# Kernel tuning notes

Measured on AMD Instinct MI355X. Metric: run time of the kernel, lower is better.

## Reference

```python
import jax, jax.numpy as jnp
import numpy as np

L = 4096   # num_tokens (one prefill sequence)
D = 2048   # hidden_size
HK = 16    # num_k_heads
HV = 32    # num_v_heads
DK = 128   # head_k_dim
DV = 128   # head_v_dim
RATIO = HV // HK
EPS = 1e-6


def setup_inputs() -> dict:
    key = jax.random.key(0)
    ks = jax.random.split(key, 11)
    s = 0.02
    return {
        "hidden_states": jax.random.normal(ks[0], (L, D), jnp.float32),
        "Wq": jax.random.normal(ks[1], (D, HK * DK), jnp.float32) * s,
        "Wk": jax.random.normal(ks[2], (D, HK * DK), jnp.float32) * s,
        "Wv": jax.random.normal(ks[3], (D, HV * DV), jnp.float32) * s,
        "Wz": jax.random.normal(ks[4], (D, HV * DV), jnp.float32) * s,
        "Wb": jax.random.normal(ks[5], (D, HV), jnp.float32) * s,
        "Wa": jax.random.normal(ks[6], (D, HV), jnp.float32) * s,
        "A_log": jnp.log(jax.random.uniform(ks[7], (HV,), jnp.float32, 1.0, 16.0)),
        "dt_bias": jax.random.normal(ks[8], (HV,), jnp.float32) * 0.5,
        "norm_weight": jnp.ones((DV,), jnp.float32),
        "W_out": jax.random.normal(ks[9], (HV * DV, D), jnp.float32) * s,
    }


def _l2norm(x):
    return x * jax.lax.rsqrt(jnp.sum(x * x, axis=-1, keepdims=True) + EPS)


def reference(hidden_states, Wq, Wk, Wv, Wz, Wb, Wa, A_log, dt_bias, norm_weight, W_out):
    h = hidden_states
    # --- input projections (qkvz + ba split) ---
    q = _l2norm((h @ Wq).reshape(L, HK, DK))            # [L, HK, DK]
    k = _l2norm((h @ Wk).reshape(L, HK, DK))
    v = (h @ Wv).reshape(L, HV, DV)                     # [L, HV, DV]
    z = (h @ Wz).reshape(L, HV, DV)                     # gate for RMSNorm
    beta = jax.nn.sigmoid(h @ Wb)                       # [L, HV]
    g = -jnp.exp(A_log) * jax.nn.softplus(h @ Wa + dt_bias)  # [L, HV]
    decay = jnp.exp(g)                                  # per-token per-head decay
    # repeat shared q/k heads to value heads (GQA ratio)
    q = jnp.repeat(q, RATIO, axis=1) * (DK ** -0.5)     # [L, HV, DK]
    k = jnp.repeat(k, RATIO, axis=1)

    # --- gated delta rule recurrence over tokens ---
    def step(S, xs):
        q_t, k_t, v_t, b_t, d_t = xs                    # [HV,DK],[HV,DK],[HV,DV],[HV],[HV]
        S = S * d_t[:, None, None]                      # decay state [HV, DK, DV]
        pred = jnp.einsum('hk,hkv->hv', k_t, S)         # memory readout
        delta = (v_t - pred) * b_t[:, None]             # delta-rule correction
        S = S + k_t[:, :, None] * delta[:, None, :]
        o = jnp.einsum('hk,hkv->hv', q_t, S)
        return S, o

    S0 = jnp.zeros((HV, DK, DV), jnp.float32)
    _, core = jax.lax.scan(step, S0, (q, k, v, beta, decay))  # core: [L, HV, DV]

    # --- gated RMSNorm: x * silu(z), rms-normalize over head dim ---
    x = core * jax.nn.silu(z)
    x = x * jax.lax.rsqrt(jnp.mean(x * x, axis=-1, keepdims=True) + EPS) * norm_weight

    # --- output projection ---
    return x.reshape(L, HV * DV) @ W_out                # [L, D]
```

## Files before the change

### kernel.cpp

```cpp
#include <hip/hip_runtime.h>

#define LTOK 4096
#define DHID 2048
#define HKN  16
#define HVN  32
#define DKK  128
#define NTOT 12288

typedef unsigned short u16;
typedef __attribute__((ext_vector_type(8))) short short8;
typedef __attribute__((ext_vector_type(8))) unsigned short u16x8;
typedef __attribute__((ext_vector_type(4))) unsigned short u16x4;
typedef __attribute__((ext_vector_type(4))) float f32x4;

__device__ __forceinline__ float b2f(u16 u) {
  unsigned int x = ((unsigned int)u) << 16;
  return __builtin_bit_cast(float, x);
}
__device__ __forceinline__ u16 f2bf(float f) {
  unsigned int u = __builtin_bit_cast(unsigned int, f);
  u += 0x7FFFu + ((u >> 16) & 1u);
  return (u16)(u >> 16);
}

template<int C> __device__ __forceinline__ float dppmv(float x) {
  int i = __builtin_amdgcn_update_dpp(0, __builtin_bit_cast(int, x), C, 0xF, 0xF, true);
  return __builtin_bit_cast(float, i);
}
__device__ __forceinline__ float red16(float x) {
  x += dppmv<0xB1>(x);
  x += dppmv<0x4E>(x);
  x += dppmv<0x124>(x);
  x += dppmv<0x128>(x);
  return x;
}

__device__ __forceinline__ void gld16(const void* g, void* l) {
  __builtin_amdgcn_global_load_lds((const __attribute__((address_space(1))) void*)g,
                                   (__attribute__((address_space(3))) void*)l, 16, 0, 0);
}

__device__ __forceinline__ int sw16(int r, int c, int rowc) { return (r * rowc + c) ^ ((r & 7) << 3); }

__device__ __forceinline__ void cstore(u16* C, size_t i, float v) { C[i] = f2bf(v); }
__device__ __forceinline__ void cstore(float* C, size_t i, float v) { C[i] = v; }

__global__ __launch_bounds__(256)
void k_cvt(const float* __restrict__ s, u16* __restrict__ d, int n) {
  const int i = (blockIdx.x * 256 + threadIdx.x) * 4;
  const float4 v = *(const float4*)(s + i);
  ushort4 o;
  o.x = f2bf(v.x); o.y = f2bf(v.y); o.z = f2bf(v.z); o.w = f2bf(v.w);
  *(ushort4*)(d + i) = o;
}

__global__ __launch_bounds__(256)
void k_tr(const float* __restrict__ src, u16* __restrict__ dst, int R, int C) {
  __shared__ float tl[32][33];
  const int r0 = blockIdx.y * 32, c0 = blockIdx.x * 32;
  const int tr = threadIdx.x >> 3, tc = (threadIdx.x & 7) * 4;
  const float4 v = *(const float4*)(src + (size_t)(r0 + tr) * C + c0 + tc);
  tl[tr][tc] = v.x; tl[tr][tc + 1] = v.y; tl[tr][tc + 2] = v.z; tl[tr][tc + 3] = v.w;
  __syncthreads();
  ushort4 o;
  o.x = f2bf(tl[tc + 0][tr]); o.y = f2bf(tl[tc + 1][tr]);
  o.z = f2bf(tl[tc + 2][tr]); o.w = f2bf(tl[tc + 3][tr]);
  *(ushort4*)(dst + (size_t)(c0 + tr) * R + r0 + tc) = o;
}

template<typename OutT>
__global__ __launch_bounds__(256, 2)
void k_gemm(const u16* __restrict__ A, const u16* __restrict__ Bt, OutT* __restrict__ C,
            int M, int N, int K) {
  __shared__ u16 lA[128 * 32];
  __shared__ u16 lB[128 * 32];
  const int tid = threadIdx.x;
  const int lane = tid & 63, wid = tid >> 6;
  const int nt = blockIdx.x, mt = blockIdx.y;
  const int wm = (wid >> 1) * 64, wn = (wid & 1) * 64;
  const size_t sK = (size_t)K;
  const u16* aS = A + (size_t)(mt * 128 + wid * 32 + (lane >> 2)) * sK + (lane & 3) * 8;
  const u16* bS = Bt + (size_t)(nt * 128 + wid * 32 + (lane >> 2)) * sK + (lane & 3) * 8;
  u16* lAw = lA + wid * 1024;
  u16* lBw = lB + wid * 1024;
  f32x4 acc[4][4] = {};
  const int aoff = (lane & 15) * 32 + (lane >> 4) * 8;

  for (int k0 = 0; k0 < K; k0 += 32) {
    gld16(aS + k0, lAw);
    gld16(aS + k0 + 16 * sK, lAw + 512);
    gld16(bS + k0, lBw);
    gld16(bS + k0 + 16 * sK, lBw + 512);
    __syncthreads();
    short8 af[4], bfv[4];
#pragma unroll
    for (int i = 0; i < 4; ++i) {
      af[i]  = *(const short8*)&lA[(wm + i * 16) * 32 + aoff];
      bfv[i] = *(const short8*)&lB[(wn + i * 16) * 32 + aoff];
    }
#pragma unroll
    for (int i = 0; i < 4; ++i)
#pragma unroll
      for (int j = 0; j < 4; ++j)
        acc[i][j] = __builtin_amdgcn_mfma_f32_16x16x32_bf16(af[i], bfv[j], acc[i][j], 0, 0, 0);
    __syncthreads();
  }
  const int r0 = mt * 128 + wm + (lane >> 4) * 4;
  const int c0 = nt * 128 + wn + (lane & 15);
#pragma unroll
  for (int i = 0; i < 4; ++i)
#pragma unroll
    for (int j = 0; j < 4; ++j)
#pragma unroll
      for (int e = 0; e < 4; ++e)
        cstore(C, (size_t)(r0 + i * 16 + e) * N + c0 + j * 16, acc[i][j][e]);
}

__global__ __launch_bounds__(256)
void k_ba(const float* __restrict__ h, const float* __restrict__ Wb, const float* __restrict__ Wa,
          const float* __restrict__ A_log, const float* __restrict__ dtb,
          float* __restrict__ beta, float* __restrict__ g_out) {
  const int w = threadIdx.x >> 6, lane = threadIdx.x & 63;
  const int t = blockIdx.x * 4 + w;
  const int j = lane & 31;
  const bool isB = lane < 32;
  const float* __restrict__ hr = h + (size_t)t * DHID;
  const float* Wc = isB ? Wb : Wa;
  float acc = 0.f;
  for (int kk = 0; kk < DHID; ++kk) acc = fmaf(hr[kk], Wc[(size_t)kk * HVN + j], acc);
  if (isB) {
    beta[(size_t)t * HVN + j] = 1.f / (1.f + expf(-acc));
  } else {
    float xx = acc + dtb[j];
    float sp = (xx > 20.f) ? xx : log1pf(expf(xx));
    g_out[(size_t)t * HVN + j] = -expf(A_log[j]) * sp;
  }
}

__global__ __launch_bounds__(256)
void k_l2n(u16* __restrict__ qkvz) {
  const int w = threadIdx.x >> 6, lane = threadIdx.x & 63;
  const int r = blockIdx.x * 4 + w;
  const int isK = r >> 16;
  const int rr = r & 65535;
  const int t = rr >> 4, hd = rr & 15;
  u16* p = qkvz + (size_t)t * NTOT + isK * 2048 + hd * DKK + lane * 2;
  float a = b2f(p[0]), b = b2f(p[1]);
  float ss = a * a + b * b;
  ss = red16(ss);
  ss += __shfl_xor(ss, 16);
  ss += __shfl_xor(ss, 32);
  const float sc = rsqrtf(ss + 1e-6f) * (isK ? 1.f : 0.08838834764831845f);
  p[0] = f2bf(a * sc); p[1] = f2bf(b * sc);
}

#define MFMA16(a, b, c) __builtin_amdgcn_mfma_f32_16x16x32_bf16(a, b, c, 0, 0, 0)

__global__ __launch_bounds__(256)
void k_r1(const u16* __restrict__ qkvz, const float* __restrict__ beta_g,
          const float* __restrict__ g_g, u16* __restrict__ UM_g, float* __restrict__ cumL_g) {
  const int pair = blockIdx.x;
  const int hv = pair >> 6, n = pair & 63;
  const int hk = hv >> 1;
  const int t0 = n * 64;
  const int tid = threadIdx.x, lane = tid & 63, wv = tid >> 6;
  const int fr = lane & 15, fq = lane >> 4;

  __shared__ __align__(16) u16 Xb[256 * 64];
  __shared__ __align__(16) u16 Dbuf0[64 * 64 * 2];
  __shared__ __align__(16) u16 Dbuf1[64 * 64 * 2];
  __shared__ float Lc[64];
  __shared__ float Bc[64];
  u16* Kl = Dbuf0;

  const int j = tid & 63, h = tid >> 6;
  const u16* kg = qkvz + (size_t)(t0 + j) * NTOT + 2048 + hk * DKK + h * 32;
  const u16* vg = qkvz + (size_t)(t0 + j) * NTOT + 4096 + hv * DKK + h * 32;
  u16x8 kv[4], vv[4];
#pragma unroll
  for (int i = 0; i < 4; ++i) { kv[i] = *(const u16x8*)(kg + i * 8); vv[i] = *(const u16x8*)(vg + i * 8); }
  if (tid < 64) {
    Lc[tid] = g_g[(size_t)(t0 + tid) * HVN + hv];
    Bc[tid] = beta_g[(size_t)(t0 + tid) * HVN + hv];
  }
#pragma unroll
  for (int i = 0; i < 4; ++i) *(u16x8*)&Kl[sw16(j, h * 32 + i * 8, 128)] = kv[i];
  __syncthreads();
  if (tid == 0) { float a = 0.f; for (int t = 0; t < 64; ++t) { a += Lc[t]; Lc[t] = a; } }
  __syncthreads();
  if (tid < 64) cumL_g[(size_t)pair * 64 + tid] = Lc[tid];

  {
    const float bj = Bc[j];
    const float mj = bj * __expf(Lc[j]);
#pragma unroll
    for (int i = 0; i < 4; ++i)
#pragma unroll
      for (int e = 0; e < 8; ++e) {
        int c = h * 32 + i * 8 + e;
        Xb[sw16(c, j, 64)] = f2bf(bj * b2f(vv[i][e]));
        Xb[sw16(128 + c, j, 64)] = f2bf(mj * b2f(kv[i][e]));
      }
  }
  f32x4 kk[4] = {};
#pragma unroll
  for (int ks = 0; ks < 4; ++ks) {
    short8 afr = *(const short8*)&Kl[sw16(wv * 16 + fr, ks * 32 + fq * 8, 128)];
#pragma unroll
    for (int ct = 0; ct < 4; ++ct) {
      short8 bfr = *(const short8*)&Kl[sw16(ct * 16 + fr, ks * 32 + fq * 8, 128)];
      kk[ct] = MFMA16(afr, bfr, kk[ct]);
    }
  }
  __syncthreads();

  f32x4 acc[16];
#pragma unroll
  for (int ct = 0; ct < 16; ++ct) {
    u16x4 xi = *(const u16x4*)&Xb[sw16(ct * 16 + fr, wv * 16 + fq * 4, 64)];
    acc[ct][0] = b2f(xi[0]); acc[ct][1] = b2f(xi[1]); acc[ct][2] = b2f(xi[2]); acc[ct][3] = b2f(xi[3]);
  }
#pragma unroll
  for (int ct = 0; ct < 4; ++ct) {
    const int s = ct * 16 + fr;
    u16x4 pk;
#pragma unroll
    for (int e = 0; e < 4; ++e) {
      const int t = wv * 16 + fq * 4 + e;
      float v = (s < t) ? -Bc[t] * __expf(Lc[t] - Lc[s]) * kk[ct][e] : 0.f;
      pk[e] = f2bf(v);
      Dbuf0[sw16(t, s, 64)] = pk[e];
    }
    *(u16x4*)&Dbuf0[4096 + sw16(s, wv * 16 + fq * 4, 64)] = pk;
  }
  __syncthreads();

  u16* DA = Dbuf0;
  u16* DB = Dbuf1;
  for (int stg = 0; stg < 6; ++stg) {
    u16* Dr = DA;
    u16* Dc = DA + 4096;
    short8 da0 = *(const short8*)&Dr[sw16(wv * 16 + fr, 0 + fq * 8, 64)];
    short8 da1 = *(const short8*)&Dr[sw16(wv * 16 + fr, 32 + fq * 8, 64)];
#pragma unroll
    for (int ct = 0; ct < 16; ++ct) {
      short8 b0 = *(const short8*)&Xb[sw16(ct * 16 + fr, 0 + fq * 8, 64)];
      short8 b1 = *(const short8*)&Xb[sw16(ct * 16 + fr, 32 + fq * 8, 64)];
      acc[ct] = MFMA16(da0, b0, acc[ct]);
      acc[ct] = MFMA16(da1, b1, acc[ct]);
    }
    f32x4 sq[4] = {};
    if (stg < 5) {
#pragma unroll
      for (int ct = 0; ct < 4; ++ct) {
        short8 sb0 = *(const short8*)&Dc[sw16(ct * 16 + fr, 0 + fq * 8, 64)];
        short8 sb1 = *(const short8*)&Dc[sw16(ct * 16 + fr, 32 + fq * 8, 64)];
        sq[ct] = MFMA16(da0, sb0, sq[ct]);
        sq[ct] = MFMA16(da1, sb1, sq[ct]);
      }
    }
    __syncthreads();
#pragma unroll
    for (int ct = 0; ct < 16; ++ct) {
      u16x4 pk;
      pk[0] = f2bf(acc[ct][0]); pk[1] = f2bf(acc[ct][1]); pk[2] = f2bf(acc[ct][2]); pk[3] = f2bf(acc[ct][3]);
      *(u16x4*)&Xb[sw16(ct * 16 + fr, wv * 16 + fq * 4, 64)] = pk;
    }
    if (stg < 5) {
#pragma unroll
      for (int ct = 0; ct < 4; ++ct) {
        u16x4 pk;
        pk[0] = f2bf(sq[ct][0]); pk[1] = f2bf(sq[ct][1]); pk[2] = f2bf(sq[ct][2]); pk[3] = f2bf(sq[ct][3]);
        *(u16x4*)&(DB + 4096)[sw16(ct * 16 + fr, wv * 16 + fq * 4, 64)] = pk;
#pragma unroll
        for (int e = 0; e < 4; ++e) DB[sw16(wv * 16 + fq * 4 + e, ct * 16 + fr, 64)] = pk[e];
      }
    }
    __syncthreads();
    u16* tmp = DA; DA = DB; DB = tmp;
  }

#pragma unroll
  for (int ct = 0; ct < 16; ++ct) {
    const int c = ct * 16 + fr;
#pragma unroll
    for (int e = 0; e < 4; ++e) {
      const int t = wv * 16 + fq * 4 + e;
      float v = acc[ct][e];
      if (ct >= 8) v = -v;
      UM_g[((size_t)pair * 64 + t) * 256 + c] = f2bf(v);
    }
  }
}

__global__ __launch_bounds__(512)
void k_r2(u16* __restrict__ qkvz, const u16* __restrict__ UM_g,
          const float* __restrict__ cumL_g, u16* __restrict__ o1_g) {
  const int hv = blockIdx.x >> 1, cs = blockIdx.x & 1;
  const int hk = hv >> 1;
  const int tid = threadIdx.x, lane = tid & 63, w = tid >> 6;
  const int fr = lane & 15, fq = lane >> 4;
  const int j = tid & 63, h = tid >> 6;

  __shared__ __align__(16) u16 Ml2[2][8192];
  __shared__ __align__(16) u16 Ql2[2][8192];
  __shared__ __align__(16) u16 Kt2[2][8192];
  __shared__ __align__(16) u16 Ul2[2][4096];
  __shared__ __align__(16) u16 dT[4096];
  __shared__ __align__(16) u16 SbT[8192];
  __shared__ __align__(16) u16 o1b[4096];
  __shared__ float Lc2[2][64];

  const int tw = w & 3;
  const int d0 = (w >> 2) * 2;

  f32x4 sacc[4];
#pragma unroll
  for (int d = 0; d < 4; ++d) sacc[d] = (f32x4){0.f, 0.f, 0.f, 0.f};
  for (int i = tid; i < 8192; i += 512) SbT[i] = 0;

  u16x8 pQ0, pQ1, pK0, pK1, pM0, pM1, pU0;
  float pL, pL63;

#define PREF(nn) {                                                            \
    const int nc = ((nn) < 64) ? (nn) : 63;                                   \
    const int pr = hv * 64 + nc; const int tt0 = nc * 64;                     \
    const u16* qg = qkvz + (size_t)(tt0 + j) * NTOT + hk * DKK + h * 16;      \
    pQ0 = *(const u16x8*)qg;          pQ1 = *(const u16x8*)(qg + 8);          \
    pK0 = *(const u16x8*)(qg + 2048); pK1 = *(const u16x8*)(qg + 2056);       \
    const u16* mg = UM_g + ((size_t)pr * 64 + j) * 256;                       \
    pM0 = *(const u16x8*)(mg + 128 + h * 16);                                 \
    pM1 = *(const u16x8*)(mg + 136 + h * 16);                                 \
    pU0 = *(const u16x8*)(mg + cs * 64 + h * 8);                              \
    pL = cumL_g[(size_t)pr * 64 + j]; pL63 = cumL_g[(size_t)pr * 64 + 63]; }

#define STW(b) {                                                              \
    *(u16x8*)&Ql2[b][sw16(j, h * 16, 128)] = pQ0;                             \
    *(u16x8*)&Ql2[b][sw16(j, h * 16 + 8, 128)] = pQ1;                         \
    *(u16x8*)&Ml2[b][sw16(j, h * 16, 128)] = pM0;                             \
    *(u16x8*)&Ml2[b][sw16(j, h * 16 + 8, 128)] = pM1;                         \
    const float scK = __expf(pL63 - pL);                                      \
    _Pragma("unroll")                                                         \
    for (int e = 0; e < 8; ++e) {                                             \
      Kt2[b][sw16(h * 16 + e, j, 64)] = f2bf(scK * b2f(pK0[e]));              \
      Kt2[b][sw16(h * 16 + 8 + e, j, 64)] = f2bf(scK * b2f(pK1[e]));          \
      Ul2[b][sw16(h * 8 + e, j, 64)] = pU0[e];                                \
    }                                                                         \
    if (h == 0) Lc2[b][j] = pL; }

  PREF(0)
  STW(0)
  __syncthreads();

  for (int n = 0; n < 64; ++n) {
    const int cur = n & 1;
    const int pair = hv * 64 + n, t0 = n * 64;
    const float curL63 = pL63;
    PREF(n + 1)

    short8 amf[4], aqf[4];
#pragma unroll
    for (int ks = 0; ks < 4; ++ks) {
      amf[ks] = *(const short8*)&Ml2[cur][sw16(tw * 16 + fr, ks * 32 + fq * 8, 128)];
      aqf[ks] = *(const short8*)&Ql2[cur][sw16(tw * 16 + fr, ks * 32 + fq * 8, 128)];
    }
    float el[4];
#pragma unroll
    for (int e = 0; e < 4; ++e) el[e] = __expf(Lc2[cur][tw * 16 + fq * 4 + e]);
#pragma unroll
    for (int dd = 0; dd < 2; ++dd) {
      const int d = d0 + dd;
      u16x4 uv = *(const u16x4*)&Ul2[cur][sw16(d * 16 + fr, tw * 16 + fq * 4, 64)];
      f32x4 dc;
      dc[0] = b2f(uv[0]); dc[1] = b2f(uv[1]); dc[2] = b2f(uv[2]); dc[3] = b2f(uv[3]);
      f32x4 oc = {};
#pragma unroll
      for (int ks = 0; ks < 4; ++ks) {
        short8 bs = *(const short8*)&SbT[sw16(d * 16 + fr, ks * 32 + fq * 8, 128)];
        dc = MFMA16(amf[ks], bs, dc);
        oc = MFMA16(aqf[ks], bs, oc);
      }
      u16x4 pk;
      pk[0] = f2bf(dc[0]); pk[1] = f2bf(dc[1]); pk[2] = f2bf(dc[2]); pk[3] = f2bf(dc[3]);
      *(u16x4*)&dT[sw16(d * 16 + fr, tw * 16 + fq * 4, 64)] = pk;
#pragma unroll
      for (int e = 0; e < 4; ++e)
        o1b[sw16(tw * 16 + fq * 4 + e, d * 16 + fr, 64)] = f2bf(oc[e] * el[e]);
    }
    __syncthreads();

    {
      const int i = tid * 8;
      u16x8 vd = *(const u16x8*)&dT[i];
      const int f = cs * 4096 + i;
      *(u16x8*)(qkvz + (size_t)(t0 + (f >> 7)) * NTOT + 4096 + hv * DKK + (f & 127)) = vd;
      u16x8 vo = *(const u16x8*)&o1b[i];
      *(u16x8*)(o1_g + (size_t)pair * 8192 + (size_t)(i >> 6) * 128 + cs * 64 + (i & 63)) = vo;
    }
    STW(cur ^ 1)
    {
      const float eC = __expf(curL63);
      short8 ak0 = *(const short8*)&Kt2[cur][sw16(w * 16 + fr, fq * 8, 64)];
      short8 ak1 = *(const short8*)&Kt2[cur][sw16(w * 16 + fr, 32 + fq * 8, 64)];
#pragma unroll
      for (int d = 0; d < 4; ++d) {
        short8 bd0 = *(const short8*)&dT[sw16(d * 16 + fr, fq * 8, 64)];
        short8 bd1 = *(const short8*)&dT[sw16(d * 16 + fr, 32 + fq * 8, 64)];
        f32x4 sa = sacc[d];
#pragma unroll
        for (int e = 0; e < 4; ++e) sa[e] *= eC;
        sa = MFMA16(ak0, bd0, sa);
        sa = MFMA16(ak1, bd1, sa);
        sacc[d] = sa;
        u16x4 pk;
        pk[0] = f2bf(sa[0]); pk[1] = f2bf(sa[1]); pk[2] = f2bf(sa[2]); pk[3] = f2bf(sa[3]);
        *(u16x4*)&SbT[sw16(d * 16 + fr, w * 16 + fq * 4, 128)] = pk;
      }
    }
    __syncthreads();
  }
#undef PREF
#undef STW
}

__global__ __launch_bounds__(512)
void k_r3(const u16* __restrict__ qkvz, const u16* __restrict__ o1_g,
          const float* __restrict__ cumL_g, const float* __restrict__ nw,
          u16* __restrict__ x) {
  const int pair = blockIdx.x, hv = pair >> 6, n = pair & 63, hk = hv >> 1, t0 = n * 64;
  const int tid = threadIdx.x, lane = tid & 63, w = tid >> 6;
  const int fr = lane & 15, fq = lane >> 4;
  const int j = tid & 63, h = tid >> 6;

  __shared__ __align__(16) u16 Ql[8192];
  __shared__ __align__(16) u16 Kl[8192];
  __shared__ __align__(16) u16 Gl[4096];
  __shared__ __align__(16) u16 dTl[8192];
  __shared__ __align__(16) float of[64 * 132];
  __shared__ float Lc[64];
  __shared__ float Lw[128];

  {
    const u16* qg = qkvz + (size_t)(t0 + j) * NTOT + hk * DKK + h * 16;
    u16x8 q0 = *(const u16x8*)qg, q1 = *(const u16x8*)(qg + 8);
    u16x8 k0 = *(const u16x8*)(qg + 2048), k1 = *(const u16x8*)(qg + 2056);
    *(u16x8*)&Ql[sw16(j, h * 16, 128)] = q0;
    *(u16x8*)&Ql[sw16(j, h * 16 + 8, 128)] = q1;
    *(u16x8*)&Kl[sw16(j, h * 16, 128)] = k0;
    *(u16x8*)&Kl[sw16(j, h * 16 + 8, 128)] = k1;
  }
#pragma unroll
  for (int it = 0; it < 2; ++it) {
    const int f = ((w * 2 + it) * 64 + lane) * 8;
    gld16(qkvz + (size_t)(t0 + (f >> 7)) * NTOT + 4096 + hv * DKK + (f & 127),
          (char*)dTl + (w * 2 + it) * 1024);
  }
  if (tid < 64) Lc[tid] = cumL_g[(size_t)pair * 64 + tid];
  if (tid < 128) Lw[tid] = nw[tid];
  __syncthreads();

  const int tw = w & 3, sp = (w >> 2) * 2;
  {
    f32x4 kk0 = {}, kk1 = {};
#pragma unroll
    for (int ks = 0; ks < 4; ++ks) {
      short8 aq = *(const short8*)&Ql[sw16(tw * 16 + fr, ks * 32 + fq * 8, 128)];
      short8 b0 = *(const short8*)&Kl[sw16(sp * 16 + fr, ks * 32 + fq * 8, 128)];
      short8 b1 = *(const short8*)&Kl[sw16((sp + 1) * 16 + fr, ks * 32 + fq * 8, 128)];
      kk0 = MFMA16(aq, b0, kk0);
      kk1 = MFMA16(aq, b1, kk1);
    }
#pragma unroll
    for (int e = 0; e < 4; ++e) {
      const int t = tw * 16 + fq * 4 + e;
      const float Lt = Lc[t];
      const int s0 = sp * 16 + fr, s1 = s0 + 16;
      Gl[sw16(t, s0, 64)] = f2bf((s0 <= t) ? kk0[e] * __expf(Lt - Lc[s0]) : 0.f);
      Gl[sw16(t, s1, 64)] = f2bf((s1 <= t) ? kk1[e] * __expf(Lt - Lc[s1]) : 0.f);
    }
  }
  __syncthreads();

  {
    short8 ag0 = *(const short8*)&Gl[sw16(tw * 16 + fr, fq * 8, 64)];
    short8 ag1 = *(const short8*)&Gl[sw16(tw * 16 + fr, 32 + fq * 8, 64)];
#pragma unroll
    for (int dd = 0; dd < 4; ++dd) {
      const int d = (w >> 2) * 4 + dd;
      short8 bd0 = *(const short8*)&dTl[sw16(d * 16 + fr, fq * 8, 64)];
      short8 bd1 = *(const short8*)&dTl[sw16(d * 16 + fr, 32 + fq * 8, 64)];
      f32x4 oc = {};
      oc = MFMA16(ag0, bd0, oc);
      oc = MFMA16(ag1, bd1, oc);
#pragma unroll
      for (int e = 0; e < 4; ++e) of[(tw * 16 + fq * 4 + e) * 132 + d * 16 + fr] = oc[e];
    }
  }
  __syncthreads();

  {
    const int t = tid >> 3, q8 = tid & 7;
    const u16* zp = qkvz + (size_t)(t0 + t) * NTOT + 8192 + hv * DKK + q8 * 16;
    const u16* op = o1_g + (size_t)pair * 8192 + t * 128;
    float xv[16];
    float ss = 0.f;
#pragma unroll
    for (int i = 0; i < 2; ++i) {
      u16x8 zv = *(const u16x8*)(zp + i * 8);
      u16x8 ov = *(const u16x8*)(op + (((q8 * 16 + i * 8) ^ ((t & 7) << 3))));
#pragma unroll
      for (int e = 0; e < 8; ++e) {
        float z = b2f(zv[e]);
        float o = of[t * 132 + q8 * 16 + i * 8 + e] + b2f(ov[e]);
        float xx = o * (z / (1.f + __expf(-z)));
        xv[i * 8 + e] = xx;
        ss = fmaf(xx, xx, ss);
      }
    }
    ss += __shfl_xor(ss, 1);
    ss += __shfl_xor(ss, 2);
    ss += __shfl_xor(ss, 4);
    const float scl = rsqrtf(ss * (1.f / 128.f) + 1e-6f);
    u16* xo = x + (size_t)(t0 + t) * 4096 + hv * DKK + q8 * 16;
#pragma unroll
    for (int i = 0; i < 2; ++i) {
      u16x8 pk;
#pragma unroll
      for (int e = 0; e < 8; ++e) pk[e] = f2bf(xv[i * 8 + e] * scl * Lw[q8 * 16 + i * 8 + e]);
      *(u16x8*)(xo + i * 8) = pk;
    }
  }
}

extern "C" void kernel_launch(void* const* d_in, const int* in_sizes, int n_in,
                              void* d_out, int out_size, void* d_ws, size_t ws_size,
                              hipStream_t stream) {
  const float* h    = (const float*)d_in[0];
  const float* Wq   = (const float*)d_in[1];
  const float* Wk   = (const float*)d_in[2];
  const float* Wv   = (const float*)d_in[3];
  const float* Wz   = (const float*)d_in[4];
  const float* Wb   = (const float*)d_in[5];
  const float* Wa   = (const float*)d_in[6];
  const float* Alog = (const float*)d_in[7];
  const float* dtb  = (const float*)d_in[8];
  const float* nw   = (const float*)d_in[9];
  const float* Wo   = (const float*)d_in[10];
  char* ws = (char*)d_ws;
  u16* h_bf  = (u16*)(ws);
  u16* Wt    = (u16*)(ws + 16777216ull);
  u16* UM    = (u16*)(ws);
  u16* Wto   = (u16*)(ws + 67108864ull);
  u16* qkvz  = (u16*)(ws + 83886080ull);
  u16* o1g   = (u16*)(ws + 184549376ull);
  u16* xbuf  = (u16*)(ws + 16777216ull);
  float* beta  = (float*)(ws + 218103808ull);
  float* g     = (float*)(ws + 218103808ull + 524288ull);
  float* cumL  = (float*)(ws + 218103808ull + 1048576ull);

  k_cvt<<<8192, 256, 0, stream>>>(h, h_bf, LTOK * DHID);
  k_tr<<<dim3(64, 64), 256, 0, stream>>>(Wq, Wt, 2048, 2048);
  k_tr<<<dim3(64, 64), 256, 0, stream>>>(Wk, Wt + 2048ull * 2048, 2048, 2048);
  k_tr<<<dim3(128, 64), 256, 0, stream>>>(Wv, Wt + 4096ull * 2048, 2048, 4096);
  k_tr<<<dim3(128, 64), 256, 0, stream>>>(Wz, Wt + 8192ull * 2048, 2048, 4096);
  k_tr<<<dim3(64, 128), 256, 0, stream>>>(Wo, Wto, 4096, 2048);
  k_gemm<u16><<<dim3(96, 32), 256, 0, stream>>>(h_bf, Wt, qkvz, 4096, 12288, 2048);
  k_ba<<<1024, 256, 0, stream>>>(h, Wb, Wa, Alog, dtb, beta, g);
  k_l2n<<<32768, 256, 0, stream>>>(qkvz);
  k_r1<<<2048, 256, 0, stream>>>(qkvz, beta, g, UM, cumL);
  k_r2<<<64, 512, 0, stream>>>(qkvz, UM, cumL, o1g);
  k_r3<<<2048, 512, 0, stream>>>(qkvz, o1g, cumL, nw, xbuf);
  k_gemm<float><<<dim3(16, 32), 256, 0, stream>>>(xbuf, Wto, (float*)d_out, 4096, 2048, 4096);
}
```

Measured before the change: 917.8 us.

## Replace GEMM with 256x256-tile, 4-stage async-prefetch pipelined kernel

Replaces the 128x128 single-buffered GEMM with a 512-thread kernel computing 256x256 tiles. K-tiles are prefetched three ahead into a 4-deep LDS ring using async global-to-LDS loads and explicit vmcnt waits, and MFMA blocks run at raised priority. A grid swizzle groups blocks for L2 reuse. The goal is to hide load latency and raise arithmetic intensity in the two projection GEMMs. The trade-off is much higher LDS and register use, and the output GEMM now launches only 128 blocks, which may underfill the GPU.

```diff
diff --git a/kernel.cpp b/kernel.cpp
--- a/kernel.cpp
+++ b/kernel.cpp
@@ -68,47 +68,70 @@
   *(ushort4*)(dst + (size_t)(c0 + tr) * R + r0 + tc) = o;
 }
 
+#define MFMA16(a, b, c) __builtin_amdgcn_mfma_f32_16x16x32_bf16(a, b, c, 0, 0, 0)
+
 template<typename OutT>
-__global__ __launch_bounds__(256, 2)
-void k_gemm(const u16* __restrict__ A, const u16* __restrict__ Bt, OutT* __restrict__ C,
-            int M, int N, int K) {
-  __shared__ u16 lA[128 * 32];
-  __shared__ u16 lB[128 * 32];
+__global__ __launch_bounds__(512, 2)
+void k_g256(const u16* __restrict__ A, const u16* __restrict__ Bt, OutT* __restrict__ C,
+            int M, int N, int K, int NT) {
+  __shared__ u16 Lds[4][16384];
   const int tid = threadIdx.x;
-  const int lane = tid & 63, wid = tid >> 6;
-  const int nt = blockIdx.x, mt = blockIdx.y;
-  const int wm = (wid >> 1) * 64, wn = (wid & 1) * 64;
+  const int lane = tid & 63, w = tid >> 6;
+  const int fr = lane & 15, fq = lane >> 4;
+  const int wm = (w >> 2) * 128, wn = (w & 3) * 64;
+  const int nkt = K >> 5;
   const size_t sK = (size_t)K;
-  const u16* aS = A + (size_t)(mt * 128 + wid * 32 + (lane >> 2)) * sK + (lane & 3) * 8;
-  const u16* bS = Bt + (size_t)(nt * 128 + wid * 32 + (lane >> 2)) * sK + (lane & 3) * 8;
-  u16* lAw = lA + wid * 1024;
-  u16* lBw = lB + wid * 1024;
-  f32x4 acc[4][4] = {};
-  const int aoff = (lane & 15) * 32 + (lane >> 4) * 8;
-
-  for (int k0 = 0; k0 < K; k0 += 32) {
-    gld16(aS + k0, lAw);
-    gld16(aS + k0 + 16 * sK, lAw + 512);
-    gld16(bS + k0, lBw);
-    gld16(bS + k0 + 16 * sK, lBw + 512);
-    __syncthreads();
-    short8 af[4], bfv[4];
-#pragma unroll
-    for (int i = 0; i < 4; ++i) {
-      af[i]  = *(const short8*)&lA[(wm + i * 16) * 32 + aoff];
-      bfv[i] = *(const short8*)&lB[(wn + i * 16) * 32 + aoff];
-    }
-#pragma unroll
-    for (int i = 0; i < 4; ++i)
+
+  const int cpx = gridDim.x >> 3;
+  const int swz = (blockIdx.x & 7) * cpx + (blockIdx.x >> 3);
+  const int nt = swz % NT, mt = swz / NT;
+
+  const u16* aS = A + (size_t)(mt * 256 + (tid >> 2)) * sK + (tid & 3) * 8;
+  const u16* bS = Bt + (size_t)(nt * 256 + (tid >> 2)) * sK + (tid & 3) * 8;
+
+  f32x4 acc[8][4] = {};
+
+#define STAGE(kt_) {                                                          \
+    const int sk = ((kt_) < nkt) ? (kt_) : (nkt - 1);                         \
+    u16* La = &Lds[(kt_) & 3][w * 512];                                       \
+    u16* Lb = &Lds[(kt_) & 3][8192 + w * 512];                                \
+    gld16(aS + (size_t)sk * 32, La);                                          \
+    gld16(aS + 128 * sK + (size_t)sk * 32, La + 4096);                        \
+    gld16(bS + (size_t)sk * 32, Lb);                                          \
+    gld16(bS + 128 * sK + (size_t)sk * 32, Lb + 4096); }
+
+  STAGE(0)
+  STAGE(1)
+  STAGE(2)
+
+  for (int kt = 0; kt < nkt; ++kt) {
+    STAGE(kt + 3)
+    asm volatile("s_waitcnt vmcnt(12)" ::: "memory");
+    __builtin_amdgcn_s_barrier();
+    const u16* Lc = Lds[kt & 3];
+    short8 af[8], bf[4];
+#pragma unroll
+    for (int i = 0; i < 8; ++i)
+      af[i] = *(const short8*)&Lc[(wm + i * 16 + fr) * 32 + fq * 8];
+#pragma unroll
+    for (int j = 0; j < 4; ++j)
+      bf[j] = *(const short8*)&Lc[8192 + (wn + j * 16 + fr) * 32 + fq * 8];
+    asm volatile("s_waitcnt lgkmcnt(0)" ::: "memory");
+    __builtin_amdgcn_s_barrier();
+    __builtin_amdgcn_s_setprio(1);
+#pragma unroll
+    for (int i = 0; i < 8; ++i)
 #pragma unroll
       for (int j = 0; j < 4; ++j)
-        acc[i][j] = __builtin_amdgcn_mfma_f32_16x16x32_bf16(af[i], bfv[j], acc[i][j], 0, 0, 0);
-    __syncthreads();
-  }
-  const int r0 = mt * 128 + wm + (lane >> 4) * 4;
-  const int c0 = nt * 128 + wn + (lane & 15);
-#pragma unroll
-  for (int i = 0; i < 4; ++i)
+        acc[i][j] = MFMA16(af[i], bf[j], acc[i][j]);
+    __builtin_amdgcn_s_setprio(0);
+  }
+#undef STAGE
+
+  const int r0 = mt * 256 + wm + fq * 4;
+  const int c0 = nt * 256 + wn + fr;
+#pragma unroll
+  for (int i = 0; i < 8; ++i)
 #pragma unroll
     for (int j = 0; j < 4; ++j)
 #pragma unroll
@@ -153,8 +176,6 @@
   const float sc = rsqrtf(ss + 1e-6f) * (isK ? 1.f : 0.08838834764831845f);
   p[0] = f2bf(a * sc); p[1] = f2bf(b * sc);
 }
-
-#define MFMA16(a, b, c) __builtin_amdgcn_mfma_f32_16x16x32_bf16(a, b, c, 0, 0, 0)
 
 __global__ __launch_bounds__(256)
 void k_r1(const u16* __restrict__ qkvz, const float* __restrict__ beta_g,
@@ -564,11 +585,11 @@
   k_tr<<<dim3(128, 64), 256, 0, stream>>>(Wv, Wt + 4096ull * 2048, 2048, 4096);
   k_tr<<<dim3(128, 64), 256, 0, stream>>>(Wz, Wt + 8192ull * 2048, 2048, 4096);
   k_tr<<<dim3(64, 128), 256, 0, stream>>>(Wo, Wto, 4096, 2048);
-  k_gemm<u16><<<dim3(96, 32), 256, 0, stream>>>(h_bf, Wt, qkvz, 4096, 12288, 2048);
+  k_g256<u16><<<768, 512, 0, stream>>>(h_bf, Wt, qkvz, 4096, 12288, 2048, 48);
   k_ba<<<1024, 256, 0, stream>>>(h, Wb, Wa, Alog, dtb, beta, g);
   k_l2n<<<32768, 256, 0, stream>>>(qkvz);
   k_r1<<<2048, 256, 0, stream>>>(qkvz, beta, g, UM, cumL);
   k_r2<<<64, 512, 0, stream>>>(qkvz, UM, cumL, o1g);
   k_r3<<<2048, 512, 0, stream>>>(qkvz, o1g, cumL, nw, xbuf);
-  k_gemm<float><<<dim3(16, 32), 256, 0, stream>>>(xbuf, Wto, (float*)d_out, 4096, 2048, 4096);
-}
+  k_g256<float><<<128, 512, 0, stream>>>(xbuf, Wto, (float*)d_out, 4096, 2048, 4096, 8);
+}
```

After: 932.7 us. No clear change (+1.6%).
